# Kernel tuning notes

Measured on AMD Instinct MI355X. Metric: run time of the kernel, lower is better.

## Reference

```python
import math
import jax, jax.numpy as jnp
import numpy as np

D_MODEL = 512
HEAD = 8
D_K = D_MODEL // HEAD
N_BUCKETS = 128
ROUNDS = 4
BIG = 1000000000.0


def look_back(x, zeros=True):
    # x: [b, n_chunks, chunk, ...] -> [b, n_chunks, 2*chunk, ...]
    pad_shape = (x.shape[0], 1) + x.shape[2:]
    if zeros:
        pad = jnp.zeros(pad_shape, x.dtype)
    else:
        pad = jnp.full(pad_shape, 1000000000, x.dtype)
    p = jnp.concatenate([pad, x], axis=1)
    return jnp.concatenate([p[:, :-1], p[:, 1:]], axis=2)


def setup_inputs() -> dict:
    key = jax.random.key(0)
    ks = jax.random.split(key, 8)
    B, L = 2, 4096
    query = jax.random.normal(ks[0], (B, L, D_MODEL), jnp.float32)
    value = jax.random.normal(ks[1], (B, L, D_MODEL), jnp.float32)
    mask = jnp.ones((B, L), dtype=bool)
    s = 1.0 / math.sqrt(D_MODEL)
    Wq = jax.random.normal(ks[2], (D_MODEL, D_MODEL), jnp.float32) * s
    bq = jnp.zeros((D_MODEL,), jnp.float32)
    Wv = jax.random.normal(ks[3], (D_MODEL, D_MODEL), jnp.float32) * s
    bv = jnp.zeros((D_MODEL,), jnp.float32)
    Wo = jax.random.normal(ks[4], (D_MODEL, D_MODEL), jnp.float32) * s
    bo = jnp.zeros((D_MODEL,), jnp.float32)
    # random LSH projection (module draws it per call; fixed here for determinism)
    rand_matrix = jax.random.uniform(ks[5], (D_K, ROUNDS, N_BUCKETS // 2), jnp.float32)
    return {"query": query, "value": value, "mask": mask, "Wq": Wq, "bq": bq,
            "Wv": Wv, "bv": bv, "Wo": Wo, "bo": bo, "rand_matrix": rand_matrix}


def lsh_attention(q, v, mask, rand_matrix):
    b, head, L, d_k = q.shape
    bh = b * head
    nb2 = N_BUCKETS // 2
    bl = L // N_BUCKETS
    R = ROUNDS
    # normalize queries, hash them
    q = q / jnp.linalg.norm(q, axis=-1, keepdims=True)
    fq = q.reshape(bh, L, d_k)
    rm = rand_matrix / jnp.linalg.norm(rand_matrix, axis=-1, keepdims=True)
    proj = jnp.einsum('bli,irk->blrk', fq, rm)                 # [bh,L,R,nb2]
    hashes = jnp.argmax(jnp.concatenate([proj, -proj], axis=-1), axis=-1)  # [bh,L,R]
    hash_indices = jnp.argsort(hashes, axis=1)                 # sorted order per round
    sorted_hashes = jnp.take_along_axis(hashes, hash_indices, axis=1)
    # gather queries into sorted order, chunk into buckets of 2*bl
    idx_qd = jnp.broadcast_to(hash_indices[:, :, None, :], (bh, L, d_k, R))
    rq = jnp.take_along_axis(jnp.broadcast_to(fq[:, :, :, None], (bh, L, d_k, R)), idx_qd, axis=1)
    rq = rq.reshape(bh, nb2, 2 * bl, d_k, R)
    lbk = look_back(rq)                                        # [bh,nb2,4bl,d_k,R]
    scores = jnp.einsum('bcidr,bcjdr->bcijr', rq, lbk) / math.sqrt(d_k)
    scores = scores.reshape(bh, L, 4 * bl, R)
    # padding mask
    m = jnp.broadcast_to(mask[:, None, :, None], (b, head, L, R)).reshape(bh, L, R)
    rmask = jnp.take_along_axis(m, hash_indices, axis=1).reshape(bh, nb2, 2 * bl, R)
    lbm = look_back(rmask, zeros=True)                         # pad -> False
    fm = jnp.broadcast_to(lbm[:, :, None, :, :], (bh, nb2, 2 * bl, 4 * bl, R)).reshape(bh, L, 4 * bl, R)
    scores = scores - (~fm).astype(scores.dtype) * BIG
    # same-hash mask
    sh = sorted_hashes.reshape(bh, nb2, 2 * bl, R)
    lbh = look_back(sh, zeros=False)
    heq = (sh[:, :, :, None, :] == lbh[:, :, None, :, :]).reshape(bh, L, 4 * bl, R)
    scores = scores - (~heq).astype(scores.dtype) * BIG
    # causal + self masks on original positions
    qi = hash_indices.reshape(bh, nb2, 2 * bl, R)
    ki = look_back(qi, zeros=False)
    causal = (qi[:, :, :, None, :] < ki[:, :, None, :, :]).reshape(bh, L, 4 * bl, R)
    scores = scores - causal.astype(scores.dtype) * BIG
    ieq = (qi[:, :, :, None, :] == ki[:, :, None, :, :]).reshape(bh, L, 4 * bl, R)
    scores = scores - ieq.astype(scores.dtype) * 100000.0
    # scatter scores back to original query order, correct duplicate keys across rounds
    original_indices = jnp.argsort(hash_indices, axis=1)
    score_indices = jnp.broadcast_to(original_indices[:, :, None, :], (bh, L, 4 * bl, R))
    fki = jnp.broadcast_to(ki[:, :, None, :, :], (bh, nb2, 2 * bl, 4 * bl, R)).reshape(bh, L, 4 * bl, R)
    rki = jnp.take_along_axis(fki, score_indices, axis=1)
    counts = [jnp.ones(rki.shape[:-1], jnp.int32) for _ in range(R)]
    for i in range(R - 1):
        for j in range(R - 1 - i):  # faithfully mirrors original indexing (incl. its j-offset)
            comp = (rki[..., i] == rki[..., i + 1 + j]).astype(jnp.int32)
            counts[i] = counts[i] + comp
            counts[j] = counts[j] + comp
    count_repeat_key = jnp.stack(counts, axis=-1)
    scores = jnp.take_along_axis(scores, score_indices, axis=1)
    scores = scores - jnp.log(count_repeat_key.astype(scores.dtype))
    p_attn = jax.nn.softmax(scores.reshape(bh, L, 4 * bl * R), axis=-1)
    # gather values into sorted order
    fv = v.reshape(bh, L, d_k)
    rv = jnp.take_along_axis(jnp.broadcast_to(fv[:, :, :, None], (bh, L, d_k, R)), idx_qd, axis=1)
    rv = rv.reshape(bh, nb2, 2 * bl, d_k, R)
    lbv = look_back(rv)                                        # [bh,nb2,4bl,d_k,R]
    attn_indices = jnp.broadcast_to(hash_indices[:, :, None, :], (bh, L, 4 * bl, R)).reshape(bh, L, 4 * bl * R)
    rp = jnp.take_along_axis(p_attn, attn_indices, axis=1).reshape(bh, nb2, 2 * bl, 4 * bl, R)
    out = jnp.einsum('bcikr,bckdr->bcidr', rp, lbv).reshape(bh, L, d_k, R)
    oi = jnp.broadcast_to(original_indices[:, :, None, :], (bh, L, d_k, R))
    out = jnp.take_along_axis(out, oi, axis=1).sum(axis=-1)
    return out.reshape(b, head, L, d_k)


def reference(query, value, mask, Wq, bq, Wv, bv, Wo, bo, rand_matrix):
    B, L, _ = query.shape
    q = (query @ Wq.T + bq).reshape(B, L, HEAD, D_K).transpose(0, 2, 1, 3)
    v = (value @ Wv.T + bv).reshape(B, L, HEAD, D_K).transpose(0, 2, 1, 3)
    x = lsh_attention(q, v, mask, rand_matrix)
    x = x.transpose(0, 2, 1, 3).reshape(B, L, HEAD * D_K)
    return x @ Wo.T + bo
```

## Files before the change

kernel.cpp:

```cpp
#include <hip/hip_runtime.h>

#define L4   4096
#define DK   64
#define NR   4
#define NB   128
#define WIN  128
#define DM   512
#define BH   16
#define BIGF 1000000000.0f

typedef short v8s __attribute__((ext_vector_type(8)));
typedef float v4f __attribute__((ext_vector_type(4)));

__device__ __forceinline__ unsigned short f2bf(float x) {
  union { float f; unsigned u; } v; v.f = x;
  const unsigned r = (v.u + 0x7FFFu + ((v.u >> 16) & 1u)) >> 16;
  return (unsigned short)r;
}
__device__ __forceinline__ float bf2f(unsigned short u) {
  union { unsigned u; float f; } v; v.u = ((unsigned)u) << 16;
  return v.f;
}
__device__ __forceinline__ ushort4 f2bf4(const float4 x) {
  ushort4 r; r.x = f2bf(x.x); r.y = f2bf(x.y); r.z = f2bf(x.z); r.w = f2bf(x.w);
  return r;
}

__device__ float g_fqn[(size_t)BH * L4 * DK];
__device__ unsigned short g_fqb[(size_t)BH * L4 * DK];
__device__ unsigned short g_fvb[(size_t)BH * L4 * DK];
__device__ float g_rmnT[NR * 64 * DK];
__device__ int   g_hash [BH * NR * L4];
__device__ int   g_sidx [BH * NR * L4];
__device__ int   g_shash[BH * NR * L4];
__device__ int   g_inv  [BH * NR * L4];
__device__ unsigned char g_cnt[(size_t)BH * NR * L4 * WIN];
__device__ float2 g_stat[BH * NR * L4];
__device__ float2 g_MZ  [BH * L4];
__device__ unsigned short g_p[(size_t)BH * NR * L4 * WIN];
__device__ unsigned short g_osortb[(size_t)BH * NR * L4 * DK];
__device__ unsigned short g_xb[(size_t)2 * L4 * DM];

__global__ __launch_bounds__(256) void qproj_gemm(const float* __restrict__ A,
                                                  const float* __restrict__ W,
                                                  const float* __restrict__ bias)
{
  const int m0 = blockIdx.x * 64;
  const int n0 = blockIdx.y * 64;
  __shared__ float As[32][68];
  __shared__ float Bs[32][68];
  __shared__ float red[4][64];
  __shared__ float nrm[64];
  const int tid = threadIdx.x;
  const int tm = tid & 15, tn = tid >> 4;
  const int lrow = tid >> 2, lk = (tid & 3) * 8;
  const float* arow = A + (size_t)(m0 + lrow) * DM + lk;
  const float* brow = W + (size_t)(n0 + lrow) * DM + lk;
  float4 pa0 = *(const float4*)(arow);
  float4 pa1 = *(const float4*)(arow + 4);
  float4 pb0 = *(const float4*)(brow);
  float4 pb1 = *(const float4*)(brow + 4);
  float acc[4][4] = {};
  for (int kt = 0; kt < DM; kt += 32) {
    __syncthreads();
    As[lk + 0][lrow] = pa0.x; As[lk + 1][lrow] = pa0.y; As[lk + 2][lrow] = pa0.z; As[lk + 3][lrow] = pa0.w;
    As[lk + 4][lrow] = pa1.x; As[lk + 5][lrow] = pa1.y; As[lk + 6][lrow] = pa1.z; As[lk + 7][lrow] = pa1.w;
    Bs[lk + 0][lrow] = pb0.x; Bs[lk + 1][lrow] = pb0.y; Bs[lk + 2][lrow] = pb0.z; Bs[lk + 3][lrow] = pb0.w;
    Bs[lk + 4][lrow] = pb1.x; Bs[lk + 5][lrow] = pb1.y; Bs[lk + 6][lrow] = pb1.z; Bs[lk + 7][lrow] = pb1.w;
    __syncthreads();
    if (kt + 32 < DM) {
      pa0 = *(const float4*)(arow + kt + 32);
      pa1 = *(const float4*)(arow + kt + 36);
      pb0 = *(const float4*)(brow + kt + 32);
      pb1 = *(const float4*)(brow + kt + 36);
    }
    #pragma unroll
    for (int kk = 0; kk < 32; ++kk) {
      const float4 av = *(const float4*)&As[kk][tm * 4];
      const float4 bv = *(const float4*)&Bs[kk][tn * 4];
      const float am[4] = {av.x, av.y, av.z, av.w};
      const float bn[4] = {bv.x, bv.y, bv.z, bv.w};
      #pragma unroll
      for (int a = 0; a < 4; ++a)
        #pragma unroll
        for (int b = 0; b < 4; ++b)
          acc[a][b] = fmaf(am[a], bn[b], acc[a][b]);
    }
  }
  #pragma unroll
  for (int b = 0; b < 4; ++b) {
    const float bb = bias[n0 + tn * 4 + b];
    #pragma unroll
    for (int a = 0; a < 4; ++a) acc[a][b] += bb;
  }
  const int lane = tid & 63, w4 = tid >> 6;
  float sq[4];
  #pragma unroll
  for (int a = 0; a < 4; ++a) {
    float s = acc[a][0] * acc[a][0];
    s = fmaf(acc[a][1], acc[a][1], s);
    s = fmaf(acc[a][2], acc[a][2], s);
    s = fmaf(acc[a][3], acc[a][3], s);
    s += __shfl_xor(s, 16);
    s += __shfl_xor(s, 32);
    sq[a] = s;
  }
  if ((lane >> 4) == 0) {
    #pragma unroll
    for (int a = 0; a < 4; ++a) red[w4][tm * 4 + a] = sq[a];
  }
  __syncthreads();
  if (tid < 64) {
    const float t = red[0][tid] + red[1][tid] + red[2][tid] + red[3][tid];
    nrm[tid] = 1.0f / sqrtf(t);
  }
  __syncthreads();
  const int bh = (m0 >> 12) * 8 + (n0 >> 6);
  const int lb = m0 & (L4 - 1);
  #pragma unroll
  for (int a = 0; a < 4; ++a) {
    const float sc = nrm[tm * 4 + a];
    const size_t idx = ((size_t)bh * L4 + lb + tm * 4 + a) * DK + tn * 4;
    float4 o;
    o.x = acc[a][0] * sc; o.y = acc[a][1] * sc;
    o.z = acc[a][2] * sc; o.w = acc[a][3] * sc;
    *(float4*)(g_fqn + idx) = o;
    *(ushort4*)(g_fqb + idx) = f2bf4(o);
  }
}

template<int MODE>
__global__ __launch_bounds__(256) void mgemm(const float* __restrict__ Af,
                                             const float* __restrict__ W,
                                             const float* __restrict__ bias,
                                             float* __restrict__ outp)
{
  const int m0 = blockIdx.x * 128;
  const int n0 = blockIdx.y * 64;
  __shared__ unsigned short As[128][72];
  __shared__ unsigned short Bs[64][72];
  const int tid = threadIdx.x;
  const int lane = tid & 63, w = tid >> 6;
  const int li = lane & 15, lq = lane >> 4;
  v4f acc[2][4];
  #pragma unroll
  for (int mt = 0; mt < 2; ++mt)
    #pragma unroll
    for (int jt = 0; jt < 4; ++jt) acc[mt][jt] = (v4f){0.f, 0.f, 0.f, 0.f};
  for (int kt = 0; kt < DM; kt += 64) {
    __syncthreads();
    {
      const int row = tid >> 1, h = tid & 1;
      if constexpr (MODE == 1) {
        const float* src = Af + (size_t)(m0 + row) * DM + kt + h * 32;
        #pragma unroll
        for (int u = 0; u < 4; ++u) {
          const float4 x = *(const float4*)(src + u * 8);
          const float4 y = *(const float4*)(src + u * 8 + 4);
          *(ushort4*)&As[row][h * 32 + u * 8]     = f2bf4(x);
          *(ushort4*)&As[row][h * 32 + u * 8 + 4] = f2bf4(y);
        }
      } else {
        const unsigned short* src = g_xb + (size_t)(m0 + row) * DM + kt + h * 32;
        #pragma unroll
        for (int u = 0; u < 4; ++u)
          *(uint4*)&As[row][h * 32 + u * 8] = ((const uint4*)src)[u];
      }
    }
    {
      const int row = tid >> 2, p = tid & 3;
      const float* src = W + (size_t)(n0 + row) * DM + kt + p * 16;
      #pragma unroll
      for (int u = 0; u < 2; ++u) {
        const float4 x = *(const float4*)(src + u * 8);
        const float4 y = *(const float4*)(src + u * 8 + 4);
        *(ushort4*)&Bs[row][p * 16 + u * 8]     = f2bf4(x);
        *(ushort4*)&Bs[row][p * 16 + u * 8 + 4] = f2bf4(y);
      }
    }
    __syncthreads();
    #pragma unroll
    for (int ks = 0; ks < 2; ++ks) {
      const v8s aq0 = *(const v8s*)&As[w * 32 + li][ks * 32 + lq * 8];
      const v8s aq1 = *(const v8s*)&As[w * 32 + 16 + li][ks * 32 + lq * 8];
      #pragma unroll
      for (int jt = 0; jt < 4; ++jt) {
        const v8s bk = *(const v8s*)&Bs[jt * 16 + li][ks * 32 + lq * 8];
        acc[0][jt] = __builtin_amdgcn_mfma_f32_16x16x32_bf16(aq0, bk, acc[0][jt], 0, 0, 0);
        acc[1][jt] = __builtin_amdgcn_mfma_f32_16x16x32_bf16(aq1, bk, acc[1][jt], 0, 0, 0);
      }
    }
  }
  #pragma unroll
  for (int mt = 0; mt < 2; ++mt)
    #pragma unroll
    for (int jt = 0; jt < 4; ++jt)
      #pragma unroll
      for (int reg = 0; reg < 4; ++reg) {
        const int m = m0 + w * 32 + mt * 16 + lq * 4 + reg;
        const int n = n0 + jt * 16 + li;
        const float vv = acc[mt][jt][reg] + bias[n];
        if constexpr (MODE == 1) {
          const int bh = (m >> 12) * 8 + (n >> 6);
          const int l = m & (L4 - 1);
          g_fvb[((size_t)bh * L4 + l) * DK + (n & 63)] = f2bf(vv);
        } else {
          outp[(size_t)m * DM + n] = vv;
        }
      }
}

__global__ __launch_bounds__(64) void rmnorm_kernel(const float* __restrict__ rm) {
  const int dr = blockIdx.x;
  const int k = threadIdx.x;
  const float v = rm[dr * 64 + k];
  float s = v * v;
  #pragma unroll
  for (int off = 32; off; off >>= 1) s += __shfl_xor(s, off);
  const int d = dr >> 2, r = dr & 3;
  g_rmnT[(r * 64 + k) * DK + d] = v / sqrtf(s);
}

__global__ __launch_bounds__(256, 4) void hash_kernel() {
  const int tid = threadIdx.x;
  const int w = __builtin_amdgcn_readfirstlane(tid >> 6);
  const int lane = tid & 63;
  const int row = blockIdx.x * 64 + lane;
  float q[64];
  #pragma unroll
  for (int du = 0; du < 16; ++du) {
    const float4 v = *(const float4*)(g_fqn + (size_t)row * DK + du * 4);
    q[du * 4 + 0] = v.x; q[du * 4 + 1] = v.y;
    q[du * 4 + 2] = v.z; q[du * 4 + 3] = v.w;
  }
  const float* rmw = g_rmnT + w * (64 * DK);
  float bestP = -BIGF, bestN = -BIGF;
  int idxP = 0, idxN = 0;
  for (int k = 0; k < 64; k += 2) {
    const float* rp0 = rmw + k * DK;
    const float* rp1 = rp0 + DK;
    float a0 = 0.f, a1 = 0.f;
    #pragma unroll
    for (int d = 0; d < 64; ++d) {
      a0 = fmaf(q[d], rp0[d], a0);
      a1 = fmaf(q[d], rp1[d], a1);
    }
    if (a0 > bestP)  { bestP = a0;  idxP = k; }
    if (-a0 > bestN) { bestN = -a0; idxN = k; }
    if (a1 > bestP)  { bestP = a1;  idxP = k + 1; }
    if (-a1 > bestN) { bestN = -a1; idxN = k + 1; }
  }
  const int idx = (bestP >= bestN) ? idxP : 64 + idxN;
  const int bh = row >> 12, l = row & (L4 - 1);
  g_hash[(bh * NR + w) * L4 + l] = idx;
}

__global__ __launch_bounds__(128) void sort_kernel() {
  __shared__ int chunkHist[64][NB];
  __shared__ int tot[NB];
  __shared__ int binBase[NB];
  const int bhr = blockIdx.x;
  const int t = threadIdx.x;
  const int* hrow = g_hash + bhr * L4;
  for (int idx = t; idx < 64 * NB; idx += 128) ((int*)chunkHist)[idx] = 0;
  __syncthreads();
  if (t < 64) {
    for (int e = 0; e < 64; ++e) chunkHist[t][hrow[t * 64 + e]]++;
  }
  __syncthreads();
  if (t < NB) { int s = 0; for (int cc = 0; cc < 64; ++cc) s += chunkHist[cc][t]; tot[t] = s; }
  __syncthreads();
  if (t == 0) { int run = 0; for (int h = 0; h < NB; ++h) { binBase[h] = run; run += tot[h]; } }
  __syncthreads();
  if (t < NB) {
    int run = binBase[t];
    for (int cc = 0; cc < 64; ++cc) { const int tmp = chunkHist[cc][t]; chunkHist[cc][t] = run; run += tmp; }
  }
  __syncthreads();
  if (t < 64) {
    for (int e = 0; e < 64; ++e) {
      const int l = t * 64 + e;
      const int h = hrow[l];
      const int p = chunkHist[t][h]++;
      g_sidx [bhr * L4 + p] = l;
      g_shash[bhr * L4 + p] = h;
      g_inv  [bhr * L4 + l] = p;
    }
  }
}

__global__ __launch_bounds__(256) void counts_kernel() {
  const int bh = blockIdx.x;
  const int l0 = blockIdx.y * 32;
  const int j = threadIdx.x & 127;
  const int lh = threadIdx.x >> 7;
  for (int u = 0; u < 16; ++u) {
    const int l = l0 + u * 2 + lh;
    int a[4];
    #pragma unroll
    for (int r = 0; r < NR; ++r) {
      const int base = (bh * NR + r) * L4;
      const int spos = g_inv[base + l];
      const int c = spos >> 6;
      a[r] = (c == 0 && j < 64) ? (1 << 20) : g_sidx[base + c * 64 - 64 + j];
    }
    const int c01 = a[0] == a[1], c02 = a[0] == a[2], c03 = a[0] == a[3];
    const int c12 = a[1] == a[2], c13 = a[1] == a[3], c23 = a[2] == a[3];
    const unsigned char n0 = (unsigned char)(1 + 2 * c01 + c02 + c03 + c12 + c23);
    const unsigned char n1 = (unsigned char)(1 + c02 + c12 + 2 * c13);
    const unsigned char n2 = (unsigned char)(1 + c03 + c23);
    g_cnt[((size_t)(bh * NR + 0) * L4 + l) * WIN + j] = n0;
    g_cnt[((size_t)(bh * NR + 1) * L4 + l) * WIN + j] = n1;
    g_cnt[((size_t)(bh * NR + 2) * L4 + l) * WIN + j] = n2;
    g_cnt[((size_t)(bh * NR + 3) * L4 + l) * WIN + j] = 1;
  }
}

__global__ __launch_bounds__(256) void passA_kernel() {
  const int c = blockIdx.x, r = blockIdx.y, bh = blockIdx.z;
  const int base = (bh * NR + r) * L4;
  const int s0 = c * 64;
  __shared__ unsigned short QKP[13824];
  __shared__ unsigned char cnt8[64][128];
  __shared__ int qi_s[64], qh_s[64], ki_s[128], kh_s[128];
  __shared__ float lutl[9];
  unsigned short (*Qb)[72] = (unsigned short(*)[72])QKP;
  unsigned short (*Kb)[72] = (unsigned short(*)[72])(QKP + 64 * 72);
  unsigned short (*Pt)[136] = (unsigned short(*)[136])QKP;
  const int tid = threadIdx.x;
  if (tid < 9) lutl[tid] = __logf((float)(tid < 1 ? 1 : tid));
  {
    const int i = tid >> 2, p = tid & 3;
    const int qi = g_sidx[base + s0 + i];
    if (p == 0) { qi_s[i] = qi; qh_s[i] = g_shash[base + s0 + i]; }
    const uint4* src = (const uint4*)(g_fqb + ((size_t)bh * L4 + qi) * DK);
    *(uint4*)&Qb[i][p * 16]     = src[2 * p];
    *(uint4*)&Qb[i][p * 16 + 8] = src[2 * p + 1];
    const uint4* cs = (const uint4*)(g_cnt + (size_t)(base + qi) * WIN);
    *(uint4*)&cnt8[i][p * 32]      = cs[2 * p];
    *(uint4*)&cnt8[i][p * 32 + 16] = cs[2 * p + 1];
  }
  {
    const int j = tid >> 1, h = tid & 1;
    const bool pad = (c == 0) && (j < 64);
    if (pad) {
      if (h == 0) { ki_s[j] = -1; kh_s[j] = (1 << 30); }
      const uint4 z = make_uint4(0, 0, 0, 0);
      #pragma unroll
      for (int u = 0; u < 4; ++u) *(uint4*)&Kb[j][h * 32 + u * 8] = z;
    } else {
      const int ki = g_sidx[base + s0 - 64 + j];
      if (h == 0) { ki_s[j] = ki; kh_s[j] = g_shash[base + s0 - 64 + j]; }
      const uint4* src = (const uint4*)(g_fqb + ((size_t)bh * L4 + ki) * DK);
      #pragma unroll
      for (int u = 0; u < 4; ++u) *(uint4*)&Kb[j][h * 32 + u * 8] = src[h * 4 + u];
    }
  }
  __syncthreads();
  const int lane = tid & 63, w = tid >> 6;
  const int i0 = w * 16;
  const int li = lane & 15, lq = lane >> 4;
  v4f acc[8];
  #pragma unroll
  for (int jt = 0; jt < 8; ++jt) acc[jt] = (v4f){0.f, 0.f, 0.f, 0.f};
  #pragma unroll
  for (int ks = 0; ks < 2; ++ks) {
    const v8s aq = *(const v8s*)&Qb[i0 + li][ks * 32 + lq * 8];
    #pragma unroll
    for (int jt = 0; jt < 8; ++jt) {
      const v8s bk = *(const v8s*)&Kb[jt * 16 + li][ks * 32 + lq * 8];
      acc[jt] = __builtin_amdgcn_mfma_f32_16x16x32_bf16(aq, bk, acc[jt], 0, 0, 0);
    }
  }
  float mrow[4], zrow[4];
  #pragma unroll
  for (int reg = 0; reg < 4; ++reg) {
    const int i = i0 + lq * 4 + reg;
    const int qi = qi_s[i], qh = qh_s[i];
    float lm = -3.0f * BIGF;
    #pragma unroll
    for (int jt = 0; jt < 8; ++jt) {
      const int j = jt * 16 + li;
      const int ki = ki_s[j], kh = kh_s[j];
      float s;
      if (ki < 0) {
        s = 0.f - BIGF - BIGF - BIGF;
      } else {
        s = acc[jt][reg] * 0.125f;
        if (qh != kh) s -= BIGF;
        if (qi < ki)  s -= BIGF;
        if (qi == ki) s -= 100000.0f;
        s -= lutl[cnt8[i][j]];
      }
      acc[jt][reg] = s;
      lm = fmaxf(lm, s);
    }
    #pragma unroll
    for (int off = 1; off < 16; off <<= 1) lm = fmaxf(lm, __shfl_xor(lm, off));
    mrow[reg] = lm;
    float ps = 0.f;
    #pragma unroll
    for (int jt = 0; jt < 8; ++jt) ps += __expf(acc[jt][reg] - lm);
    #pragma unroll
    for (int off = 1; off < 16; off <<= 1) ps += __shfl_xor(ps, off);
    zrow[reg] = ps;
    if (li == 0) g_stat[base + s0 + i] = make_float2(lm, ps);
  }
  __syncthreads();
  #pragma unroll
  for (int reg = 0; reg < 4; ++reg) {
    const int i = i0 + lq * 4 + reg;
    #pragma unroll
    for (int jt = 0; jt < 8; ++jt)
      Pt[i][jt * 16 + li] = f2bf(__expf(acc[jt][reg] - mrow[reg]));
  }
  __syncthreads();
  unsigned short* gp = g_p + ((size_t)(base + s0)) * WIN;
  #pragma unroll
  for (int it = 0; it < 4; ++it) {
    const int t = tid + it * 256;
    const int row = t >> 4, colu = t & 15;
    ((uint4*)gp)[t] = *(const uint4*)&Pt[row][colu * 8];
  }
}

__global__ __launch_bounds__(256) void merge_kernel() {
  const int idx = blockIdx.x * 256 + threadIdx.x;
  const int bh = idx >> 12, l = idx & (L4 - 1);
  float m[4], z[4];
  #pragma unroll
  for (int r = 0; r < NR; ++r) {
    const int base = (bh * NR + r) * L4;
    const int spos = g_inv[base + l];
    const float2 st = g_stat[base + spos];
    m[r] = st.x; z[r] = st.y;
  }
  const float M = fmaxf(fmaxf(m[0], m[1]), fmaxf(m[2], m[3]));
  const float Z = z[0] * __expf(m[0] - M) + z[1] * __expf(m[1] - M)
                + z[2] * __expf(m[2] - M) + z[3] * __expf(m[3] - M);
  g_MZ[idx] = make_float2(M, 1.0f / Z);
}

__global__ __launch_bounds__(256) void passB_kernel() {
  const int c = blockIdx.x, r = blockIdx.y, bh = blockIdx.z;
  const int base = (bh * NR + r) * L4;
  const int s0 = c * 64;
  __shared__ unsigned short Pb[64][136];
  __shared__ unsigned short Vt[64][136];
  __shared__ float scale_s[64];
  const int tid = threadIdx.x;
  const unsigned short* gp = g_p + ((size_t)(base + s0)) * WIN;
  #pragma unroll
  for (int it = 0; it < 4; ++it) {
    const int t = tid + it * 256;
    const int row = t >> 4, colu = t & 15;
    *(uint4*)&Pb[row][colu * 8] = ((const uint4*)gp)[t];
  }
  if (tid < 64) {
    const float m_r = g_stat[base + s0 + tid].x;
    const int qi = g_sidx[base + s0 + tid];
    const float2 mz = g_MZ[(size_t)bh * L4 + qi];
    scale_s[tid] = __expf(m_r - mz.x) * mz.y;
  }
  {
    const int j = tid >> 1, h = tid & 1;
    const bool pad = (c == 0) && (j < 64);
    if (pad) {
      #pragma unroll
      for (int d = 0; d < 32; ++d) Vt[h * 32 + d][j] = 0;
    } else {
      const int ki = g_sidx[base + s0 - 64 + j];
      const uint4* src = (const uint4*)(g_fvb + ((size_t)bh * L4 + ki) * DK);
      #pragma unroll
      for (int u = 0; u < 4; ++u) {
        const uint4 v = src[h * 4 + u];
        const unsigned short* e = (const unsigned short*)&v;
        #pragma unroll
        for (int t = 0; t < 8; ++t) Vt[h * 32 + u * 8 + t][j] = e[t];
      }
    }
  }
  __syncthreads();
  const int lane = tid & 63, w = tid >> 6;
  const int i0 = w * 16;
  const int li = lane & 15, lq = lane >> 4;
  v4f acc[4];
  #pragma unroll
  for (int dt = 0; dt < 4; ++dt) acc[dt] = (v4f){0.f, 0.f, 0.f, 0.f};
  #pragma unroll
  for (int ks = 0; ks < 4; ++ks) {
    const v8s pa = *(const v8s*)&Pb[i0 + li][ks * 32 + lq * 8];
    #pragma unroll
    for (int dt = 0; dt < 4; ++dt) {
      const v8s vb = *(const v8s*)&Vt[dt * 16 + li][ks * 32 + lq * 8];
      acc[dt] = __builtin_amdgcn_mfma_f32_16x16x32_bf16(pa, vb, acc[dt], 0, 0, 0);
    }
  }
  #pragma unroll
  for (int reg = 0; reg < 4; ++reg) {
    const int i = i0 + lq * 4 + reg;
    const float sc = scale_s[i];
    unsigned short* orow = g_osortb + ((size_t)(base + s0 + i)) * DK;
    #pragma unroll
    for (int dt = 0; dt < 4; ++dt)
      orow[dt * 16 + li] = f2bf(acc[dt][reg] * sc);
  }
}

__global__ __launch_bounds__(256) void combine_kernel() {
  const int b = blockIdx.x >> 12, l = blockIdx.x & (L4 - 1);
  const int tid = threadIdx.x;
  const int d = tid & 63, h0 = tid >> 6;
  #pragma unroll
  for (int hh = h0; hh < 8; hh += 4) {
    const int bh = b * 8 + hh;
    float v = 0.f;
    #pragma unroll
    for (int r = 0; r < NR; ++r) {
      const int s = g_inv[(bh * NR + r) * L4 + l];
      v += bf2f(g_osortb[((size_t)(bh * NR + r) * L4 + s) * DK + d]);
    }
    g_xb[((size_t)b * L4 + l) * DM + hh * 64 + d] = f2bf(v);
  }
}

extern "C" void kernel_launch(void* const* d_in, const int* in_sizes, int n_in,
                              void* d_out, int out_size, void* d_ws, size_t ws_size,
                              hipStream_t stream) {
  (void)in_sizes; (void)n_in; (void)d_ws; (void)ws_size; (void)out_size;
  const float* query = (const float*)d_in[0];
  const float* value = (const float*)d_in[1];
  const float* Wq = (const float*)d_in[3];
  const float* bq = (const float*)d_in[4];
  const float* Wv = (const float*)d_in[5];
  const float* bv = (const float*)d_in[6];
  const float* Wo = (const float*)d_in[7];
  const float* bo = (const float*)d_in[8];
  const float* rm = (const float*)d_in[9];
  float* out = (float*)d_out;

  qproj_gemm<<<dim3(128, 8), 256, 0, stream>>>(query, Wq, bq);
  mgemm<1><<<dim3(64, 8), 256, 0, stream>>>(value, Wv, bv, nullptr);
  rmnorm_kernel<<<256, 64, 0, stream>>>(rm);
  hash_kernel<<<1024, 256, 0, stream>>>();
  sort_kernel<<<64, 128, 0, stream>>>();
  counts_kernel<<<dim3(16, 128), 256, 0, stream>>>();
  passA_kernel<<<dim3(64, 4, 16), 256, 0, stream>>>();
  merge_kernel<<<256, 256, 0, stream>>>();
  passB_kernel<<<dim3(64, 4, 16), 256, 0, stream>>>();
  combine_kernel<<<8192, 256, 0, stream>>>();
  mgemm<2><<<dim3(64, 8), 256, 0, stream>>>(nullptr, Wo, bo, out);
}
```

Baseline: 293.9 us.

## Enlarge Q-projection GEMM tile to 128 rows with 8x4 register tiles

The fp32 Q projection GEMM now uses 128x64 output tiles with an 8x4 per-thread micro-tile instead of 64x64 with 4x4. Each thread now owns whole rows' worth of a 16-lane group, so the row norm is reduced with lane shuffles only, and the shared-memory reduction and its two barriers are gone. This raises arithmetic intensity per shared-memory load but halves the grid to 512 blocks and increases register use, which may lower occupancy.

```diff
diff --git a/kernel.cpp b/kernel.cpp
--- a/kernel.cpp
+++ b/kernel.cpp
@@ -45,85 +45,84 @@
                                                   const float* __restrict__ W,
                                                   const float* __restrict__ bias)
 {
-  const int m0 = blockIdx.x * 64;
+  const int m0 = blockIdx.x * 128;
   const int n0 = blockIdx.y * 64;
-  __shared__ float As[32][68];
+  __shared__ float As[32][132];
   __shared__ float Bs[32][68];
-  __shared__ float red[4][64];
-  __shared__ float nrm[64];
   const int tid = threadIdx.x;
-  const int tm = tid & 15, tn = tid >> 4;
-  const int lrow = tid >> 2, lk = (tid & 3) * 8;
-  const float* arow = A + (size_t)(m0 + lrow) * DM + lk;
-  const float* brow = W + (size_t)(n0 + lrow) * DM + lk;
+  const int am = tid & 127, ak0 = (tid >> 7) * 16;
+  const int bn = tid & 63,  bk0 = (tid >> 6) * 8;
+  const float* arow = A + (size_t)(m0 + am) * DM + ak0;
+  const float* brow = W + (size_t)(n0 + bn) * DM + bk0;
   float4 pa0 = *(const float4*)(arow);
   float4 pa1 = *(const float4*)(arow + 4);
+  float4 pa2 = *(const float4*)(arow + 8);
+  float4 pa3 = *(const float4*)(arow + 12);
   float4 pb0 = *(const float4*)(brow);
   float4 pb1 = *(const float4*)(brow + 4);
-  float acc[4][4] = {};
+  const int lane = tid & 63, w = tid >> 6;
+  const int ng = lane & 15, mgl = lane >> 4;
+  const int mbase = (w * 4 + mgl) * 8;
+  const int nbase = ng * 4;
+  float acc[8][4] = {};
   for (int kt = 0; kt < DM; kt += 32) {
     __syncthreads();
-    As[lk + 0][lrow] = pa0.x; As[lk + 1][lrow] = pa0.y; As[lk + 2][lrow] = pa0.z; As[lk + 3][lrow] = pa0.w;
-    As[lk + 4][lrow] = pa1.x; As[lk + 5][lrow] = pa1.y; As[lk + 6][lrow] = pa1.z; As[lk + 7][lrow] = pa1.w;
-    Bs[lk + 0][lrow] = pb0.x; Bs[lk + 1][lrow] = pb0.y; Bs[lk + 2][lrow] = pb0.z; Bs[lk + 3][lrow] = pb0.w;
-    Bs[lk + 4][lrow] = pb1.x; Bs[lk + 5][lrow] = pb1.y; Bs[lk + 6][lrow] = pb1.z; Bs[lk + 7][lrow] = pb1.w;
+    As[ak0 +  0][am] = pa0.x; As[ak0 +  1][am] = pa0.y; As[ak0 +  2][am] = pa0.z; As[ak0 +  3][am] = pa0.w;
+    As[ak0 +  4][am] = pa1.x; As[ak0 +  5][am] = pa1.y; As[ak0 +  6][am] = pa1.z; As[ak0 +  7][am] = pa1.w;
+    As[ak0 +  8][am] = pa2.x; As[ak0 +  9][am] = pa2.y; As[ak0 + 10][am] = pa2.z; As[ak0 + 11][am] = pa2.w;
+    As[ak0 + 12][am] = pa3.x; As[ak0 + 13][am] = pa3.y; As[ak0 + 14][am] = pa3.z; As[ak0 + 15][am] = pa3.w;
+    Bs[bk0 + 0][bn] = pb0.x; Bs[bk0 + 1][bn] = pb0.y; Bs[bk0 + 2][bn] = pb0.z; Bs[bk0 + 3][bn] = pb0.w;
+    Bs[bk0 + 4][bn] = pb1.x; Bs[bk0 + 5][bn] = pb1.y; Bs[bk0 + 6][bn] = pb1.z; Bs[bk0 + 7][bn] = pb1.w;
     __syncthreads();
     if (kt + 32 < DM) {
       pa0 = *(const float4*)(arow + kt + 32);
       pa1 = *(const float4*)(arow + kt + 36);
+      pa2 = *(const float4*)(arow + kt + 40);
+      pa3 = *(const float4*)(arow + kt + 44);
       pb0 = *(const float4*)(brow + kt + 32);
       pb1 = *(const float4*)(brow + kt + 36);
     }
     #pragma unroll
     for (int kk = 0; kk < 32; ++kk) {
-      const float4 av = *(const float4*)&As[kk][tm * 4];
-      const float4 bv = *(const float4*)&Bs[kk][tn * 4];
-      const float am[4] = {av.x, av.y, av.z, av.w};
-      const float bn[4] = {bv.x, bv.y, bv.z, bv.w};
-      #pragma unroll
-      for (int a = 0; a < 4; ++a)
+      const float4 a0 = *(const float4*)&As[kk][mbase];
+      const float4 a1 = *(const float4*)&As[kk][mbase + 4];
+      const float4 bv = *(const float4*)&Bs[kk][nbase];
+      const float amv[8] = {a0.x, a0.y, a0.z, a0.w, a1.x, a1.y, a1.z, a1.w};
+      const float bnv[4] = {bv.x, bv.y, bv.z, bv.w};
+      #pragma unroll
+      for (int i = 0; i < 8; ++i)
         #pragma unroll
-        for (int b = 0; b < 4; ++b)
-          acc[a][b] = fmaf(am[a], bn[b], acc[a][b]);
-    }
-  }
-  #pragma unroll
-  for (int b = 0; b < 4; ++b) {
-    const float bb = bias[n0 + tn * 4 + b];
-    #pragma unroll
-    for (int a = 0; a < 4; ++a) acc[a][b] += bb;
-  }
-  const int lane = tid & 63, w4 = tid >> 6;
-  float sq[4];
-  #pragma unroll
-  for (int a = 0; a < 4; ++a) {
-    float s = acc[a][0] * acc[a][0];
-    s = fmaf(acc[a][1], acc[a][1], s);
-    s = fmaf(acc[a][2], acc[a][2], s);
-    s = fmaf(acc[a][3], acc[a][3], s);
-    s += __shfl_xor(s, 16);
-    s += __shfl_xor(s, 32);
-    sq[a] = s;
-  }
-  if ((lane >> 4) == 0) {
-    #pragma unroll
-    for (int a = 0; a < 4; ++a) red[w4][tm * 4 + a] = sq[a];
-  }
-  __syncthreads();
-  if (tid < 64) {
-    const float t = red[0][tid] + red[1][tid] + red[2][tid] + red[3][tid];
-    nrm[tid] = 1.0f / sqrtf(t);
-  }
-  __syncthreads();
+        for (int j = 0; j < 4; ++j)
+          acc[i][j] = fmaf(amv[i], bnv[j], acc[i][j]);
+    }
+  }
+  #pragma unroll
+  for (int j = 0; j < 4; ++j) {
+    const float bb = bias[n0 + nbase + j];
+    #pragma unroll
+    for (int i = 0; i < 8; ++i) acc[i][j] += bb;
+  }
+  float sc[8];
+  #pragma unroll
+  for (int i = 0; i < 8; ++i) {
+    float s = acc[i][0] * acc[i][0];
+    s = fmaf(acc[i][1], acc[i][1], s);
+    s = fmaf(acc[i][2], acc[i][2], s);
+    s = fmaf(acc[i][3], acc[i][3], s);
+    s += __shfl_xor(s, 1);
+    s += __shfl_xor(s, 2);
+    s += __shfl_xor(s, 4);
+    s += __shfl_xor(s, 8);
+    sc[i] = 1.0f / sqrtf(s);
+  }
   const int bh = (m0 >> 12) * 8 + (n0 >> 6);
-  const int lb = m0 & (L4 - 1);
-  #pragma unroll
-  for (int a = 0; a < 4; ++a) {
-    const float sc = nrm[tm * 4 + a];
-    const size_t idx = ((size_t)bh * L4 + lb + tm * 4 + a) * DK + tn * 4;
+  const int lb = (m0 & (L4 - 1)) + mbase;
+  #pragma unroll
+  for (int i = 0; i < 8; ++i) {
+    const size_t idx = ((size_t)bh * L4 + lb + i) * DK + nbase;
     float4 o;
-    o.x = acc[a][0] * sc; o.y = acc[a][1] * sc;
-    o.z = acc[a][2] * sc; o.w = acc[a][3] * sc;
+    o.x = acc[i][0] * sc[i]; o.y = acc[i][1] * sc[i];
+    o.z = acc[i][2] * sc[i]; o.w = acc[i][3] * sc[i];
     *(float4*)(g_fqn + idx) = o;
     *(ushort4*)(g_fqb + idx) = f2bf4(o);
   }
@@ -539,7 +538,7 @@
   const float* rm = (const float*)d_in[9];
   float* out = (float*)d_out;
 
-  qproj_gemm<<<dim3(128, 8), 256, 0, stream>>>(query, Wq, bq);
+  qproj_gemm<<<dim3(64, 8), 256, 0, stream>>>(query, Wq, bq);
   mgemm<1><<<dim3(64, 8), 256, 0, stream>>>(value, Wv, bv, nullptr);
   rmnorm_kernel<<<256, 64, 0, stream>>>(rm);
   hash_kernel<<<1024, 256, 0, stream>>>();
```

Measured after the change: 288.8 us. No clear change (-1.7%).
